# Optimization experiments

Hardware: AMD Instinct MI355X
Metric: run time of the kernel (lower is better)

The kernel has to match this reference:

```python
import jax, jax.numpy as jnp
import numpy as np

EPS = 1e-8
ELASTICITY = jnp.array([0.05, 0.12, 0.08, 0.15, 0.10], dtype=jnp.float32)
N_SIDE = 3  # sqrt(control_points=9)


def _kernel_distance(d2):
    # kornia TPS radial basis: 0.5 * r^2 * log(r^2 + eps)
    return 0.5 * d2 * jnp.log(d2 + EPS)


def _pair_sq_dist(a, b):  # [B,N,2],[B,M,2] -> [B,N,M]
    return jnp.sum((a[:, :, None, :] - b[:, None, :, :]) ** 2, axis=-1)


def grid_sample_bilinear(img, grid):
    """F.grid_sample, mode=bilinear, padding_mode=zeros, align_corners=True.
    img [B,C,H,W], grid [B,H,W,2] with (x,y) in [-1,1]."""
    B, C, H, W = img.shape
    gx = (grid[..., 0] + 1.0) * 0.5 * (W - 1)
    gy = (grid[..., 1] + 1.0) * 0.5 * (H - 1)
    x0 = jnp.floor(gx); y0 = jnp.floor(gy)
    x1 = x0 + 1.0; y1 = y0 + 1.0
    wx1 = gx - x0; wx0 = 1.0 - wx1
    wy1 = gy - y0; wy0 = 1.0 - wy1
    b = jnp.arange(B)[:, None, None]

    def gather(yi, xi):
        valid = (xi >= 0) & (xi <= W - 1) & (yi >= 0) & (yi <= H - 1)
        xc = jnp.clip(xi, 0, W - 1).astype(jnp.int32)
        yc = jnp.clip(yi, 0, H - 1).astype(jnp.int32)
        v = img[b, :, yc, xc]  # [B,H,W,C]
        return v * valid[..., None].astype(img.dtype)

    out = (gather(y0, x0) * (wy0 * wx0)[..., None]
           + gather(y0, x1) * (wy0 * wx1)[..., None]
           + gather(y1, x0) * (wy1 * wx0)[..., None]
           + gather(y1, x1) * (wy1 * wx1)[..., None])
    return jnp.transpose(out, (0, 3, 1, 2))


def control_points_src(B):
    ii, jj = jnp.meshgrid(jnp.arange(N_SIDE, dtype=jnp.float32),
                          jnp.arange(N_SIDE, dtype=jnp.float32), indexing='ij')
    src = jnp.stack([2.0 * ii / (N_SIDE - 1) - 1.0,
                     2.0 * jj / (N_SIDE - 1) - 1.0], axis=-1).reshape(-1, 2)
    return jnp.broadcast_to(src, (B, N_SIDE * N_SIDE, 2))


def point_elasticity(masks_f):
    # masks_f [B,nc,H,W]; 5x5 window around each control point, argmax class
    H, W = masks_f.shape[2], masks_f.shape[3]
    elas = []
    for i in range(N_SIDE):
        for j in range(N_SIDE):
            y = int(i / (N_SIDE - 1) * (H - 1))
            x = int(j / (N_SIDE - 1) * (W - 1))
            y0, y1 = max(0, y - 2), min(H, y + 3)
            x0, x1 = max(0, x - 2), min(W, x + 3)
            region = masks_f[:, :, y0:y1, x0:x1].sum((2, 3))  # [B,nc]
            dom = jnp.argmax(region, axis=1)
            elas.append(ELASTICITY[dom])
    return jnp.stack(elas, axis=1)  # [B,9]


def get_tps_transform(src, dst):
    B, N, _ = src.shape
    K = _kernel_distance(_pair_sq_dist(src, src))                 # [B,N,N]
    P = jnp.concatenate([jnp.ones((B, N, 1), src.dtype), src], -1)  # [B,N,3]
    top = jnp.concatenate([K, P], axis=-1)
    bot = jnp.concatenate([jnp.swapaxes(P, 1, 2),
                           jnp.zeros((B, 3, 3), src.dtype)], axis=-1)
    L = jnp.concatenate([top, bot], axis=1)                        # [B,N+3,N+3]
    rhs = jnp.concatenate([dst, jnp.zeros((B, 3, 2), src.dtype)], axis=1)
    w = jnp.linalg.solve(L, rhs)
    return w[:, :N], w[:, N:]


def warp_image_tps(img, centers, kernel_w, affine_w):
    B, C, H, W = img.shape
    gx, gy = jnp.meshgrid(jnp.linspace(-1.0, 1.0, W), jnp.linspace(-1.0, 1.0, H))
    pts = jnp.stack([gx.ravel(), gy.ravel()], axis=-1)             # [HW,2]
    pts = jnp.broadcast_to(pts, (B, H * W, 2))
    k = _kernel_distance(_pair_sq_dist(pts, centers))              # [B,HW,N]
    pts_aug = jnp.concatenate([jnp.ones((B, H * W, 1), img.dtype), pts], -1)
    warped = k @ kernel_w + pts_aug @ affine_w                     # [B,HW,2]
    return grid_sample_bilinear(img, warped.reshape(B, H, W, 2))


def tps_transform(img, masks_f, noise):
    B = img.shape[0]
    disp = noise * point_elasticity(masks_f)[..., None]            # [B,9,2]
    # smooth the single interior control point (i=j=1 -> idx 4)
    neigh = (disp[:, 1] + disp[:, 7] + disp[:, 3] + disp[:, 5]) * 0.25
    disp = disp.at[:, 4].set(0.8 * disp[:, 4] + 0.2 * neigh)
    src = control_points_src(B)
    kw, aw = get_tps_transform(src, src + disp)
    return warp_image_tps(img, src, kw, aw)


def class_aware_mixup(x, masks_f, lam, perm):
    bg = (masks_f.sum(1, keepdims=True) == 0).astype(x.dtype)
    fg = (masks_f == 1).astype(x.dtype).sum(1, keepdims=True)
    return bg * x + fg * (lam * x + (1.0 - lam) * x[perm])


def setup_inputs() -> dict:
    key = jax.random.key(0)
    k1, k2, k3, k4, k5, k6 = jax.random.split(key, 6)
    B, H, W, NC = 128, 192, 192, 5
    return {
        'x': jax.random.normal(k1, (B, 1, H, W), dtype=jnp.float32),
        'masks': jax.random.randint(k2, (B, NC, H, W), 0, 2, dtype=jnp.int32),
        'lam': jax.random.beta(k3, 0.4, 0.4, dtype=jnp.float32),
        'perm': jax.random.permutation(k4, B).astype(jnp.int32),
        'noise_g': jax.random.normal(k5, (B, 9, 2), dtype=jnp.float32),
        'noise_l': jax.random.normal(k6, (B, 9, 2), dtype=jnp.float32),
        'epoch': 10,
        'total_epochs': 100,
    }


def reference(x, masks, lam, perm, noise_g, noise_l, epoch, total_epochs):
    masks_f = masks.astype(x.dtype)
    mixed_x = class_aware_mixup(x, masks_f, lam, perm)
    global_aug = tps_transform(mixed_x, masks_f, noise_g)
    local_aug = tps_transform(x, masks_f, noise_l)
    return (global_aug, local_aug)
```

## Files before the change

kernel.cpp:

```cpp
#include <hip/hip_runtime.h>
#include <math.h>

#define B_    128
#define H_    192
#define W_    192
#define NC_   5
#define HW_   (H_*W_)
#define NPTS  9
#define EPS_  1e-8f
#define CHUNK 8
#define MIXB  (B_*HW_/4/256)
#define LOCB  ((W_/64)*(H_/4)*(B_/CHUNK))

typedef int   vint4   __attribute__((ext_vector_type(4)));
typedef float vfloat4 __attribute__((ext_vector_type(4)));
typedef float vfloat2 __attribute__((ext_vector_type(2)));

struct LinvT { float m[12][NPTS]; };

__global__ void prep_kernel(const int* __restrict__ masks,
                            const float* __restrict__ ng,
                            const float* __restrict__ nl,
                            LinvT Linv, float* __restrict__ wts)
{
    const float ETAB[5] = {0.05f, 0.12f, 0.08f, 0.15f, 0.1f};
    __shared__ int   sums[NPTS][NC_];
    __shared__ float elas_s[NPTS];
    int b = blockIdx.x;
    int t = threadIdx.x;

    if (t < NPTS * NC_) {
        int pt = t / NC_, c = t - pt * NC_;
        int i = pt / 3, j = pt % 3;
        int yc = (i * (H_ - 1)) / 2;
        int xc = (j * (W_ - 1)) / 2;
        int y0 = yc - 2 < 0 ? 0 : yc - 2;
        int y1 = yc + 3 > H_ ? H_ : yc + 3;
        int x0 = xc - 2 < 0 ? 0 : xc - 2;
        int x1 = xc + 3 > W_ ? W_ : xc + 3;
        int s = 0;
        for (int y = y0; y < y1; ++y)
            for (int xx = x0; xx < x1; ++xx)
                s += masks[((size_t)b * NC_ + c) * HW_ + y * W_ + xx];
        sums[pt][c] = s;
    }
    __syncthreads();
    if (t < NPTS) {
        int best = -1, best_c = 0;
        #pragma unroll
        for (int c = 0; c < NC_; ++c) {
            int s = sums[t][c];
            if (s > best) { best = s; best_c = c; }
        }
        elas_s[t] = ETAB[best_c];
    }
    __syncthreads();
    if (t < 24) {
        int tr = t / 12, r = t - tr * 12;
        const float* noise = (tr == 0) ? ng : nl;
        float disp[NPTS][2];
        #pragma unroll
        for (int k = 0; k < NPTS; ++k) {
            float e = elas_s[k];
            disp[k][0] = noise[((size_t)b * NPTS + k) * 2 + 0] * e;
            disp[k][1] = noise[((size_t)b * NPTS + k) * 2 + 1] * e;
        }
        #pragma unroll
        for (int c = 0; c < 2; ++c) {
            float nb = (disp[1][c] + disp[7][c] + disp[3][c] + disp[5][c]) * 0.25f;
            disp[4][c] = 0.8f * disp[4][c] + 0.2f * nb;
        }
        float a0 = 0.f, a1 = 0.f;
        #pragma unroll
        for (int k = 0; k < NPTS; ++k) {
            float d0 = (float)(k / 3 - 1) + disp[k][0];
            float d1 = (float)(k % 3 - 1) + disp[k][1];
            a0 += Linv.m[r][k] * d0;
            a1 += Linv.m[r][k] * d1;
        }
        float* wout = wts + ((size_t)tr * B_ + b) * 24;
        wout[r * 2 + 0] = a0;
        wout[r * 2 + 1] = a1;
    }
}

__device__ __forceinline__ void tps_coords_pk(
    const vfloat2* __restrict__ wt2, float px, float py, const float* __restrict__ u,
    int& o00, int& o01, int& o10, int& o11,
    float& w00, float& w01, float& w10, float& w11)
{
    vfloat2 g = wt2[9];
    g = __builtin_elementwise_fma((vfloat2){px, px}, wt2[10], g);
    g = __builtin_elementwise_fma((vfloat2){py, py}, wt2[11], g);
    #pragma unroll
    for (int k = 0; k < NPTS; ++k)
        g = __builtin_elementwise_fma((vfloat2){u[k], u[k]}, wt2[k], g);
    const float sc = 0.5f * (float)(W_ - 1);
    float ix = fmaf(g.x, sc, sc);
    float iy = fmaf(g.y, sc, sc);
    float x0f = floorf(ix), y0f = floorf(iy);
    float wx1 = ix - x0f, wx0 = 1.f - wx1;
    float wy1 = iy - y0f, wy0 = 1.f - wy1;
    int x0 = (int)x0f, y0 = (int)y0f;
    float fx0 = ((unsigned)x0 < 192u)       ? wx0 : 0.f;
    float fx1 = ((unsigned)(x0 + 1) < 192u) ? wx1 : 0.f;
    float fy0 = ((unsigned)y0 < 192u)       ? wy0 : 0.f;
    float fy1 = ((unsigned)(y0 + 1) < 192u) ? wy1 : 0.f;
    w00 = fy0 * fx0; w01 = fy0 * fx1; w10 = fy1 * fx0; w11 = fy1 * fx1;
    int o = y0 * W_ + x0;
    o00 = min(max(o, 0), HW_ - 1);
    o01 = min(max(o + 1, 0), HW_ - 1);
    o10 = min(max(o + W_, 0), HW_ - 1);
    o11 = min(max(o + W_ + 1, 0), HW_ - 1);
}

__device__ __forceinline__ void warp_body(
    const float* __restrict__ srcb, const float* __restrict__ wts,
    float* __restrict__ out, int gx, int gy, int combo0)
{
    int tx  = threadIdx.x;
    int wpx = gx * 64 + (tx & 63);
    int h   = gy * 4 + (tx >> 6);
    int p   = h * W_ + wpx;
    float px = -1.f + wpx * (2.f / (float)(W_ - 1));
    float py = -1.f + h   * (2.f / (float)(H_ - 1));

    float u[NPTS];
    #pragma unroll
    for (int k = 0; k < NPTS; ++k) {
        float dx = px - (float)(k / 3 - 1);
        float dy = py - (float)(k % 3 - 1);
        float d2 = dx * dx + dy * dy;
        u[k] = 0.5f * d2 * __logf(d2 + EPS_);
    }

    const vfloat2* wt2base = reinterpret_cast<const vfloat2*>(wts);

    #pragma unroll
    for (int g4 = 0; g4 < CHUNK; g4 += 4) {
        int   o00[4], o01[4], o10[4], o11[4];
        float w00[4], w01[4], w10[4], w11[4];
        const float* src[4];
        #pragma unroll
        for (int q = 0; q < 4; ++q) {
            int combo = combo0 + g4 + q;
            int b = combo & (B_ - 1);
            src[q] = srcb + (size_t)b * HW_;
            tps_coords_pk(wt2base + (size_t)combo * 12, px, py, u,
                          o00[q], o01[q], o10[q], o11[q],
                          w00[q], w01[q], w10[q], w11[q]);
        }
        float v00[4], v01[4], v10[4], v11[4];
        #pragma unroll
        for (int q = 0; q < 4; ++q) {
            v00[q] = src[q][o00[q]];
            v01[q] = src[q][o01[q]];
            v10[q] = src[q][o10[q]];
            v11[q] = src[q][o11[q]];
        }
        #pragma unroll
        for (int q = 0; q < 4; ++q) {
            int combo = combo0 + g4 + q;
            float val = w00[q] * v00[q] + w01[q] * v01[q] +
                        w10[q] * v10[q] + w11[q] * v11[q];
            __builtin_nontemporal_store(val, &out[(size_t)combo * HW_ + p]);
        }
    }
}

__device__ __forceinline__ void mixup_body(
    const float* __restrict__ x, const int* __restrict__ masks,
    const float* __restrict__ lam_p, const int* __restrict__ perm,
    float* __restrict__ mixed, int mb)
{
    int idx = mb * 256 + threadIdx.x;
    float lam = lam_p[0];
    int b  = idx / (HW_ / 4);
    int p4 = (idx - b * (HW_ / 4)) * 4;
    const vfloat4 xv = *reinterpret_cast<const vfloat4*>(x + (size_t)b * HW_ + p4);
    int pb = perm[b];
    const vfloat4 xp = *reinterpret_cast<const vfloat4*>(x + (size_t)pb * HW_ + p4);

    vint4 ma[NC_];
    #pragma unroll
    for (int c = 0; c < NC_; ++c)
        ma[c] = __builtin_nontemporal_load(
            reinterpret_cast<const vint4*>(masks + ((size_t)b * NC_ + c) * HW_ + p4));
    vfloat4 outv;
    #pragma unroll
    for (int l = 0; l < 4; ++l) {
        int s = 0, fg = 0;
        #pragma unroll
        for (int c = 0; c < NC_; ++c) { int m = ma[c][l]; s += m; fg += (m == 1); }
        float bg = (s == 0) ? 1.f : 0.f;
        outv[l] = bg * xv[l] + (float)fg * (lam * xv[l] + (1.f - lam) * xp[l]);
    }
    *reinterpret_cast<vfloat4*>(mixed + (size_t)b * HW_ + p4) = outv;
}

__global__ __launch_bounds__(256, 2) void mix_local_kernel(
    const float* __restrict__ x, const int* __restrict__ masks,
    const float* __restrict__ lam_p, const int* __restrict__ perm,
    float* __restrict__ mixed, const float* __restrict__ wts,
    float* __restrict__ out)
{
    int bid   = blockIdx.x;
    int group = bid / 3;
    int r     = bid - group * 3;

    if (r < 2) {
        mixup_body(x, masks, lam_p, perm, mixed, group * 2 + r);
    } else {
        int lb = group;
        int half  = (lb >= LOCB / 2) ? 1 : 0;
        int lbh   = lb - half * (LOCB / 2);
        int gz    = (lbh & 7) + 8 * half;
        int inner = lbh >> 3;
        int gx = inner % 3, gy = inner / 3;
        warp_body(x, wts, out, gx, gy, B_ + gz * CHUNK);
    }
}

__global__ __launch_bounds__(256, 2) void warp_global_kernel(
    const float* __restrict__ mixed, const float* __restrict__ wts,
    float* __restrict__ out)
{
    int bid   = blockIdx.x;
    int gz    = bid & 15;
    int inner = bid >> 4;
    int gx = inner % 3, gy = inner / 3;
    warp_body(mixed, wts, out, gx, gy, gz * CHUNK);
}

static void build_linv(LinvT* out)
{
    double srcp[NPTS][2];
    for (int k = 0; k < NPTS; ++k) {
        srcp[k][0] = (double)(k / 3) - 1.0;
        srcp[k][1] = (double)(k % 3) - 1.0;
    }
    double A[12][24];
    for (int r = 0; r < 12; ++r)
        for (int c = 0; c < 24; ++c) A[r][c] = 0.0;
    for (int i = 0; i < NPTS; ++i) {
        for (int j = 0; j < NPTS; ++j) {
            double dx = srcp[i][0] - srcp[j][0];
            double dy = srcp[i][1] - srcp[j][1];
            double d2 = dx * dx + dy * dy;
            A[i][j] = 0.5 * d2 * log(d2 + 1e-8);
        }
        A[i][9]  = 1.0; A[i][10] = srcp[i][0]; A[i][11] = srcp[i][1];
        A[9][i]  = 1.0; A[10][i] = srcp[i][0]; A[11][i] = srcp[i][1];
    }
    for (int r = 0; r < 12; ++r) A[r][12 + r] = 1.0;
    for (int col = 0; col < 12; ++col) {
        int piv = col; double mx = fabs(A[col][col]);
        for (int r = col + 1; r < 12; ++r)
            if (fabs(A[r][col]) > mx) { mx = fabs(A[r][col]); piv = r; }
        if (piv != col)
            for (int c = 0; c < 24; ++c) { double tmp = A[col][c]; A[col][c] = A[piv][c]; A[piv][c] = tmp; }
        double d = A[col][col];
        for (int c = 0; c < 24; ++c) A[col][c] /= d;
        for (int r = 0; r < 12; ++r) {
            if (r == col) continue;
            double f = A[r][col];
            if (f != 0.0)
                for (int c = 0; c < 24; ++c) A[r][c] -= f * A[col][c];
        }
    }
    for (int r = 0; r < 12; ++r)
        for (int k = 0; k < NPTS; ++k)
            out->m[r][k] = (float)A[r][12 + k];
}

extern "C" void kernel_launch(void* const* d_in, const int* in_sizes, int n_in,
                              void* d_out, int out_size, void* d_ws, size_t ws_size,
                              hipStream_t stream)
{
    (void)in_sizes; (void)n_in; (void)out_size; (void)ws_size;
    const float* x     = (const float*)d_in[0];
    const int*   masks = (const int*)d_in[1];
    const float* lam   = (const float*)d_in[2];
    const int*   perm  = (const int*)d_in[3];
    const float* ng    = (const float*)d_in[4];
    const float* nl    = (const float*)d_in[5];
    float* out = (float*)d_out;

    char* ws = (char*)d_ws;
    float* wts   = (float*)ws;
    float* mixed = (float*)(ws + 32768);

    LinvT Linv;
    build_linv(&Linv);

    prep_kernel<<<B_, 64, 0, stream>>>(masks, ng, nl, Linv, wts);
    mix_local_kernel<<<MIXB + LOCB, 256, 0, stream>>>(
        x, masks, lam, perm, mixed, wts, out);
    warp_global_kernel<<<LOCB, 256, 0, stream>>>(mixed, wts, out);
}
```

Baseline: 56.99 us.

## Fuse three launches into one cooperative persistent kernel with grid syncs

Replaces the prep, mixup/local-warp and global-warp launches with a single cooperative kernel of 512 persistent blocks that loops over the same work items, separated by grid-wide barriers. The aim is to remove kernel launch gaps and tail effects between the three stages. The stage 1 work is spread across the persistent blocks rather than one block per item, and grid.sync adds barrier overhead. The three-launch path remains as a fallback if the cooperative launch fails.

```diff
diff --git a/kernel.cpp b/kernel.cpp
--- a/kernel.cpp
+++ b/kernel.cpp
@@ -1,4 +1,5 @@
 #include <hip/hip_runtime.h>
+#include <hip/hip_cooperative_groups.h>
 #include <math.h>
 
 #define B_    128
@@ -11,6 +12,7 @@
 #define CHUNK 8
 #define MIXB  (B_*HW_/4/256)
 #define LOCB  ((W_/64)*(H_/4)*(B_/CHUNK))
+#define COOPB 512
 
 typedef int   vint4   __attribute__((ext_vector_type(4)));
 typedef float vfloat4 __attribute__((ext_vector_type(4)));
@@ -18,15 +20,13 @@
 
 struct LinvT { float m[12][NPTS]; };
 
-__global__ void prep_kernel(const int* __restrict__ masks,
-                            const float* __restrict__ ng,
-                            const float* __restrict__ nl,
-                            LinvT Linv, float* __restrict__ wts)
+__device__ __forceinline__ void prep_body(
+    const int* __restrict__ masks, const float* __restrict__ ng,
+    const float* __restrict__ nl, const LinvT& Linv, float* __restrict__ wts, int b)
 {
     const float ETAB[5] = {0.05f, 0.12f, 0.08f, 0.15f, 0.1f};
     __shared__ int   sums[NPTS][NC_];
     __shared__ float elas_s[NPTS];
-    int b = blockIdx.x;
     int t = threadIdx.x;
 
     if (t < NPTS * NC_) {
@@ -170,11 +170,10 @@
 
 __device__ __forceinline__ void mixup_body(
     const float* __restrict__ x, const int* __restrict__ masks,
-    const float* __restrict__ lam_p, const int* __restrict__ perm,
+    float lam, const int* __restrict__ perm,
     float* __restrict__ mixed, int mb)
 {
     int idx = mb * 256 + threadIdx.x;
-    float lam = lam_p[0];
     int b  = idx / (HW_ / 4);
     int p4 = (idx - b * (HW_ / 4)) * 4;
     const vfloat4 xv = *reinterpret_cast<const vfloat4*>(x + (size_t)b * HW_ + p4);
@@ -198,6 +197,51 @@
     *reinterpret_cast<vfloat4*>(mixed + (size_t)b * HW_ + p4) = outv;
 }
 
+__global__ __launch_bounds__(256, 2) void fused_kernel(
+    const float* __restrict__ x, const int* __restrict__ masks,
+    const float* __restrict__ lam_p, const int* __restrict__ perm,
+    const float* __restrict__ ng, const float* __restrict__ nl,
+    LinvT Linv, float* __restrict__ wts, float* __restrict__ mixed,
+    float* __restrict__ out)
+{
+    cooperative_groups::grid_group grid = cooperative_groups::this_grid();
+    float lam = lam_p[0];
+
+    if (blockIdx.x < B_)
+        prep_body(masks, ng, nl, Linv, wts, blockIdx.x);
+    grid.sync();
+
+    for (int T = blockIdx.x; T < MIXB + LOCB; T += COOPB) {
+        int group = T / 3;
+        int r     = T - group * 3;
+        if (r < 2) {
+            mixup_body(x, masks, lam, perm, mixed, group * 2 + r);
+        } else {
+            int lb   = group;
+            int half = (lb >= LOCB / 2) ? 1 : 0;
+            int lbh  = lb - half * (LOCB / 2);
+            int gz   = (lbh & 7) + 8 * half;
+            int inner = lbh >> 3;
+            warp_body(x, wts, out, inner % 3, inner / 3, B_ + gz * CHUNK);
+        }
+    }
+    grid.sync();
+
+    for (int T = blockIdx.x; T < LOCB; T += COOPB) {
+        int gz    = T & 15;
+        int inner = T >> 4;
+        warp_body(mixed, wts, out, inner % 3, inner / 3, gz * CHUNK);
+    }
+}
+
+__global__ void prep_kernel(const int* __restrict__ masks,
+                            const float* __restrict__ ng,
+                            const float* __restrict__ nl,
+                            LinvT Linv, float* __restrict__ wts)
+{
+    prep_body(masks, ng, nl, Linv, wts, blockIdx.x);
+}
+
 __global__ __launch_bounds__(256, 2) void mix_local_kernel(
     const float* __restrict__ x, const int* __restrict__ masks,
     const float* __restrict__ lam_p, const int* __restrict__ perm,
@@ -207,17 +251,15 @@
     int bid   = blockIdx.x;
     int group = bid / 3;
     int r     = bid - group * 3;
-
     if (r < 2) {
-        mixup_body(x, masks, lam_p, perm, mixed, group * 2 + r);
+        mixup_body(x, masks, lam_p[0], perm, mixed, group * 2 + r);
     } else {
-        int lb = group;
-        int half  = (lb >= LOCB / 2) ? 1 : 0;
-        int lbh   = lb - half * (LOCB / 2);
-        int gz    = (lbh & 7) + 8 * half;
+        int lb   = group;
+        int half = (lb >= LOCB / 2) ? 1 : 0;
+        int lbh  = lb - half * (LOCB / 2);
+        int gz   = (lbh & 7) + 8 * half;
         int inner = lbh >> 3;
-        int gx = inner % 3, gy = inner / 3;
-        warp_body(x, wts, out, gx, gy, B_ + gz * CHUNK);
+        warp_body(x, wts, out, inner % 3, inner / 3, B_ + gz * CHUNK);
     }
 }
 
@@ -225,11 +267,9 @@
     const float* __restrict__ mixed, const float* __restrict__ wts,
     float* __restrict__ out)
 {
-    int bid   = blockIdx.x;
-    int gz    = bid & 15;
-    int inner = bid >> 4;
-    int gx = inner % 3, gy = inner / 3;
-    warp_body(mixed, wts, out, gx, gy, gz * CHUNK);
+    int gz    = blockIdx.x & 15;
+    int inner = blockIdx.x >> 4;
+    warp_body(mixed, wts, out, inner % 3, inner / 3, gz * CHUNK);
 }
 
 static void build_linv(LinvT* out)
@@ -293,8 +333,16 @@
     LinvT Linv;
     build_linv(&Linv);
 
-    prep_kernel<<<B_, 64, 0, stream>>>(masks, ng, nl, Linv, wts);
-    mix_local_kernel<<<MIXB + LOCB, 256, 0, stream>>>(
-        x, masks, lam, perm, mixed, wts, out);
-    warp_global_kernel<<<LOCB, 256, 0, stream>>>(mixed, wts, out);
-}
+    void* args[] = {(void*)&x, (void*)&masks, (void*)&lam, (void*)&perm,
+                    (void*)&ng, (void*)&nl, (void*)&Linv, (void*)&wts,
+                    (void*)&mixed, (void*)&out};
+    hipError_t err = hipLaunchCooperativeKernel(
+        (const void*)fused_kernel, dim3(COOPB), dim3(256), args, 0, stream);
+
+    if (err != hipSuccess) {
+        prep_kernel<<<B_, 64, 0, stream>>>(masks, ng, nl, Linv, wts);
+        mix_local_kernel<<<MIXB + LOCB, 256, 0, stream>>>(
+            x, masks, lam, perm, mixed, wts, out);
+        warp_global_kernel<<<LOCB, 256, 0, stream>>>(mixed, wts, out);
+    }
+}
```

After: 208.5 us. 3.66x slower.
